# Performance work log

Measured on AMD Instinct MI355X. Metric: run time of the kernel, lower is better.

The kernel has to match this reference:

```python
import jax, jax.numpy as jnp
import numpy as np

T0 = 64    # coarse proposal intervals
TF = 128   # fine samples per ray


def contract(x):
    # mip-NeRF-360 style contraction with per-point max-coordinate scatter.
    ax = jnp.abs(x)
    mag = jnp.max(ax, axis=-1, keepdims=True)             # [..., 1]
    oh = jax.nn.one_hot(jnp.argmax(ax, axis=-1), x.shape[-1], dtype=x.dtype)
    scale = (1.0 - oh) / mag + oh * (2.0 - 1.0 / mag) / mag
    return jnp.where(mag < 1.0, x, x * scale)


def near_far_from_aabb(rays_o, rays_d, aabb, min_near=0.05):
    tmin = (aabb[:3] - rays_o) / (rays_d + 1e-15)
    tmax = (aabb[3:] - rays_o) / (rays_d + 1e-15)
    near = jnp.max(jnp.minimum(tmin, tmax), axis=-1, keepdims=True)
    far = jnp.min(jnp.maximum(tmin, tmax), axis=-1, keepdims=True)
    miss = far < near
    near = jnp.where(miss, 1e9, near)
    far = jnp.where(miss, 1e9, far)
    near = jnp.maximum(near, min_near)
    return near, far


def sample_pdf(bins, weights, T):
    # CDF inverse-transform sampling (no perturb), faithful to the torch helper.
    n_int = weights.shape[-1]
    w = weights + 0.01
    pdf = w / jnp.sum(w, axis=-1, keepdims=True)
    cdf = jnp.minimum(jnp.cumsum(pdf, axis=-1), 1.0)
    cdf = jnp.concatenate([jnp.zeros_like(cdf[..., :1]), cdf], axis=-1)  # [N, n_int+1]
    u = jnp.linspace(0.5 / T, 1.0 - 0.5 / T, T, dtype=bins.dtype)
    u = jnp.broadcast_to(u, (bins.shape[0], T))
    inds = jax.vmap(lambda c, uu: jnp.searchsorted(c, uu, side='right'))(cdf, u)
    below = jnp.clip(inds - 1, 0, n_int)
    above = jnp.clip(inds, 0, n_int)
    cdf0 = jnp.take_along_axis(cdf, below, axis=-1)
    cdf1 = jnp.take_along_axis(cdf, above, axis=-1)
    b0 = jnp.take_along_axis(bins, below, axis=-1)
    b1 = jnp.take_along_axis(bins, above, axis=-1)
    denom = cdf1 - cdf0
    t = jnp.clip(jnp.where(denom > 0, (u - cdf0) / jnp.maximum(denom, 1e-12), 0.0), 0.0, 1.0)
    return b0 + t * (b1 - b0)


def setup_inputs() -> dict:
    key = jax.random.key(0)
    k1, k2, k3, k4, k5 = jax.random.split(key, 5)
    N = 65536
    rays_o = (jax.random.uniform(k1, (N, 3), jnp.float32) - 0.5) * 1.0   # origins inside box
    d = jax.random.normal(k2, (N, 3), jnp.float32)
    rays_d = d / jnp.linalg.norm(d, axis=-1, keepdims=True)
    aabb = jnp.array([-2.0, -2.0, -2.0, 2.0, 2.0, 2.0], jnp.float32)
    weights_coarse = jax.random.uniform(k3, (N, T0), jnp.float32)
    sigmas = jax.random.uniform(k4, (N, TF), jnp.float32) * 20.0
    rgbs = jax.random.uniform(k5, (N, TF, 3), jnp.float32)
    return {"rays_o": rays_o, "rays_d": rays_d, "aabb": aabb,
            "weights_coarse": weights_coarse, "sigmas": sigmas, "rgbs": rgbs}


def reference(rays_o, rays_d, aabb, weights_coarse, sigmas, rgbs):
    N = rays_o.shape[0]
    # 1) ray-AABB intersection
    near, far = near_far_from_aabb(rays_o, rays_d, aabb)
    # 2) uniform coarse bins in [near, far]
    s = jnp.linspace(0.0, 1.0, T0 + 1, dtype=rays_o.dtype)
    bins = near + (far - near) * s                              # [N, T0+1]
    # 3) CDF inverse-sample TF+1 fine bin edges from proposal weights
    z_edges = sample_pdf(bins, weights_coarse, TF + 1)          # [N, TF+1]
    deltas = z_edges[..., 1:] - z_edges[..., :-1]               # [N, TF]
    z = 0.5 * (z_edges[..., 1:] + z_edges[..., :-1])            # [N, TF]
    # 4) sample positions + contraction warp
    xyzs = rays_o[:, None, :] + rays_d[:, None, :] * z[..., None]  # [N, TF, 3]
    xyzs_c = contract(xyzs)
    # 5) alpha compositing
    alphas = 1.0 - jnp.exp(-sigmas * deltas)                    # [N, TF]
    trans = jnp.cumprod(
        jnp.concatenate([jnp.ones_like(alphas[..., :1]), 1.0 - alphas + 1e-10], axis=-1),
        axis=-1)[..., :-1]
    w = alphas * trans                                          # [N, TF]
    image = jnp.sum(w[..., None] * rgbs, axis=1)                # [N, 3]
    depth = jnp.sum(w * z, axis=-1, keepdims=True)              # [N, 1]
    return jnp.concatenate([image, depth, xyzs_c.reshape(N, -1)], axis=-1)  # [N, 4+3*TF]
```

## Files before the change

### kernel.cpp

```cpp
#include <hip/hip_runtime.h>


constexpr int kT0 = 64;
constexpr int kTF = 128;
constexpr int kRaysPerBlock = 4;

template <int Ctrl, int RowMask>
__device__ __forceinline__ float dpp_mov(float x, float oldv) {
    return __int_as_float(__builtin_amdgcn_update_dpp(
        __float_as_int(oldv), __float_as_int(x), Ctrl, RowMask, 0xf, false));
}

__device__ __forceinline__ float wave_iscan_add(float x) {
    x += dpp_mov<0x111, 0xf>(x, 0.0f);
    x += dpp_mov<0x112, 0xf>(x, 0.0f);
    x += dpp_mov<0x114, 0xf>(x, 0.0f);
    x += dpp_mov<0x118, 0xf>(x, 0.0f);
    x += dpp_mov<0x142, 0xa>(x, 0.0f);
    x += dpp_mov<0x143, 0xc>(x, 0.0f);
    return x;
}

__device__ __forceinline__ float wave_iscan_mul(float x) {
    x *= dpp_mov<0x111, 0xf>(x, 1.0f);
    x *= dpp_mov<0x112, 0xf>(x, 1.0f);
    x *= dpp_mov<0x114, 0xf>(x, 1.0f);
    x *= dpp_mov<0x118, 0xf>(x, 1.0f);
    x *= dpp_mov<0x142, 0xa>(x, 1.0f);
    x *= dpp_mov<0x143, 0xc>(x, 1.0f);
    return x;
}

template <int Dummy = 0>
__device__ __forceinline__ float wave_shr1(float x, float oldv) {
    return dpp_mov<0x138, 0xf>(x, oldv);
}

__global__ __launch_bounds__(256)
void nerf_render_kernel(const float* __restrict__ rays_o,
                        const float* __restrict__ rays_d,
                        const float* __restrict__ aabb,
                        const float* __restrict__ weights,
                        const float* __restrict__ sigmas,
                        const float* __restrict__ rgbs,
                        float* __restrict__ out)
{
    const int lane = threadIdx.x & 63;
    const int wid  = threadIdx.x >> 6;
    const int ray  = blockIdx.x * kRaysPerBlock + wid;

    __shared__ float s_zedge[kRaysPerBlock][kTF + 2];

    const float wraw = weights[(size_t)ray * kT0 + lane];
    const float2 sg  = *(const float2*)(sigmas + (size_t)ray * kTF + 2 * lane);
    const float* rgb_row = rgbs + (size_t)ray * (kTF * 3) + 6 * lane;
    const float2 rgA = *(const float2*)(rgb_row + 0);
    const float2 rgB = *(const float2*)(rgb_row + 2);
    const float2 rgC = *(const float2*)(rgb_row + 4);

    const float ox = rays_o[ray * 3 + 0], oy = rays_o[ray * 3 + 1], ozr = rays_o[ray * 3 + 2];
    const float dx = rays_d[ray * 3 + 0], dy = rays_d[ray * 3 + 1], dzr = rays_d[ray * 3 + 2];
    float near, far;
    {
        const float rx = __builtin_amdgcn_rcpf(dx + 1e-15f);
        const float ry = __builtin_amdgcn_rcpf(dy + 1e-15f);
        const float rz = __builtin_amdgcn_rcpf(dzr + 1e-15f);
        const float t0x = (aabb[0] - ox) * rx, t1x = (aabb[3] - ox) * rx;
        const float t0y = (aabb[1] - oy) * ry, t1y = (aabb[4] - oy) * ry;
        const float t0z = (aabb[2] - ozr) * rz, t1z = (aabb[5] - ozr) * rz;
        near = fmaxf(fmaxf(fminf(t0x, t1x), fminf(t0y, t1y)), fminf(t0z, t1z));
        far  = fminf(fminf(fmaxf(t0x, t1x), fmaxf(t0y, t1y)), fmaxf(t0z, t1z));
        if (far < near) { near = 1e9f; far = 1e9f; }
        near = fmaxf(near, 0.05f);
    }
    const float range = far - near;

    const float scan  = wave_iscan_add(wraw + 0.01f);
    const float total = __int_as_float(__builtin_amdgcn_readlane(__float_as_int(scan), 63));
    const float c_hi  = fminf(scan * __builtin_amdgcn_rcpf(total), 1.0f);
    const float c_lo  = wave_shr1<>(c_hi, 0.0f);

    {
        const float b_lo = near + range * ((float)lane * (1.0f / kT0));
        const float bw = range * (1.0f / kT0);
        int j_start = (int)ceilf(fmaf(129.0f, c_lo, -0.5f));
        int j_end   = (int)ceilf(fmaf(129.0f, c_hi, -0.5f));
        j_start = j_start < 0 ? 0 : j_start;
        j_end   = j_end > (kTF + 1) ? (kTF + 1) : j_end;
        const float rdenom = __builtin_amdgcn_rcpf(c_hi - c_lo);
        float fj = (float)j_start + 0.5f;
        for (int j = j_start; j < j_end; ++j, fj += 1.0f) {
            const float u = fj * (1.0f / 129.0f);
            float t = (u - c_lo) * rdenom;
            t = fminf(fmaxf(t, 0.0f), 1.0f);
            s_zedge[wid][j] = fmaf(t, bw, b_lo);
        }
    }
    __builtin_amdgcn_wave_barrier();
    __asm__ volatile("s_waitcnt lgkmcnt(0)" ::: "memory");
    __builtin_amdgcn_wave_barrier();

    const float2 ze01 = *(const float2*)&s_zedge[wid][2 * lane];
    const float  ze2  = s_zedge[wid][2 * lane + 2];
    const float d0 = ze01.y - ze01.x, d1 = ze2 - ze01.y;
    const float z0 = 0.5f * (ze01.x + ze01.y), z1 = 0.5f * (ze01.y + ze2);

    const float e0 = __expf(-sg.x * d0);
    const float e1 = __expf(-sg.y * d1);
    const float a0 = 1.0f - e0, a1 = 1.0f - e1;
    const float f0 = e0 + 1e-10f;
    const float f1 = e1 + 1e-10f;

    const float ps   = wave_iscan_mul(f0 * f1);
    const float excl = wave_shr1<>(ps, 1.0f);
    const float w0 = a0 * excl;
    const float w1 = a1 * excl * f0;

    float vr = wave_iscan_add(w0 * rgA.x + w1 * rgB.y);
    float vg = wave_iscan_add(w0 * rgA.y + w1 * rgC.x);
    float vb = wave_iscan_add(w0 * rgB.x + w1 * rgC.y);
    float vd = wave_iscan_add(w0 * z0 + w1 * z1);

    float* orow = out + (size_t)ray * (4 + kTF * 3);
    if (lane == 63) {
        *(float4*)orow = make_float4(vr, vg, vb, vd);
    }

    float oxyz[6];
    #pragma unroll
    for (int s = 0; s < 2; ++s) {
        const float z = s ? z1 : z0;
        float px = ox  + dx  * z;
        float py = oy  + dy  * z;
        float pz = ozr + dzr * z;
        const float ax = fabsf(px), ay = fabsf(py), az = fabsf(pz);
        float mag; int idx;
        if (ax >= ay && ax >= az) { mag = ax; idx = 0; }
        else if (ay >= az)        { mag = ay; idx = 1; }
        else                      { mag = az; idx = 2; }
        const float inv    = __builtin_amdgcn_rcpf(mag);
        const bool  inside = mag < 1.0f;
        const float s_oth  = inside ? 1.0f : inv;
        const float s_max  = inside ? 1.0f : (2.0f - inv) * inv;
        oxyz[3 * s + 0] = px * ((idx == 0) ? s_max : s_oth);
        oxyz[3 * s + 1] = py * ((idx == 1) ? s_max : s_oth);
        oxyz[3 * s + 2] = pz * ((idx == 2) ? s_max : s_oth);
    }
    float* o = orow + 4 + 6 * lane;
    *(float2*)(o + 0) = make_float2(oxyz[0], oxyz[1]);
    *(float2*)(o + 2) = make_float2(oxyz[2], oxyz[3]);
    *(float2*)(o + 4) = make_float2(oxyz[4], oxyz[5]);
}

extern "C" void kernel_launch(void* const* d_in, const int* in_sizes, int n_in,
                              void* d_out, int out_size, void* d_ws, size_t ws_size,
                              hipStream_t stream) {
    const float* rays_o  = (const float*)d_in[0];
    const float* rays_d  = (const float*)d_in[1];
    const float* aabb    = (const float*)d_in[2];
    const float* weights = (const float*)d_in[3];
    const float* sigmas  = (const float*)d_in[4];
    const float* rgbs    = (const float*)d_in[5];
    float* out           = (float*)d_out;

    const int N = in_sizes[0] / 3;
    const int blocks = N / kRaysPerBlock;
    nerf_render_kernel<<<blocks, 256, 0, stream>>>(rays_o, rays_d, aabb, weights, sigmas, rgbs, out);
}
```

Measured before the change: 221.1 us.

## Process multiple rays per wave with software-prefetched next-ray loads

Each wavefront now handles eight consecutive rays in an unrolled loop, loading the next ray's inputs before processing the current one, with double-buffered LDS z-edge rows. The aim is to hide global memory latency inside each wave and to amortize per-block setup such as the aabb loads. The trade-off is fewer blocks and more registers per thread, with a launch-bounds occupancy hint to keep register use in check. Less parallelism may hurt if occupancy was what hid latency before.

```diff
diff --git a/kernel.cpp b/kernel.cpp
--- a/kernel.cpp
+++ b/kernel.cpp
@@ -3,7 +3,8 @@
 
 constexpr int kT0 = 64;
 constexpr int kTF = 128;
-constexpr int kRaysPerBlock = 4;
+constexpr int kWavesPerBlock = 4;
+constexpr int kRaysPerWave = 8;
 
 template <int Ctrl, int RowMask>
 __device__ __forceinline__ float dpp_mov(float x, float oldv) {
@@ -31,43 +32,48 @@
     return x;
 }
 
-template <int Dummy = 0>
 __device__ __forceinline__ float wave_shr1(float x, float oldv) {
     return dpp_mov<0x138, 0xf>(x, oldv);
 }
 
-__global__ __launch_bounds__(256)
-void nerf_render_kernel(const float* __restrict__ rays_o,
-                        const float* __restrict__ rays_d,
-                        const float* __restrict__ aabb,
-                        const float* __restrict__ weights,
-                        const float* __restrict__ sigmas,
-                        const float* __restrict__ rgbs,
-                        float* __restrict__ out)
-{
-    const int lane = threadIdx.x & 63;
-    const int wid  = threadIdx.x >> 6;
-    const int ray  = blockIdx.x * kRaysPerBlock + wid;
-
-    __shared__ float s_zedge[kRaysPerBlock][kTF + 2];
-
-    const float wraw = weights[(size_t)ray * kT0 + lane];
-    const float2 sg  = *(const float2*)(sigmas + (size_t)ray * kTF + 2 * lane);
+struct RayIn {
+    float ox, oy, oz, dx, dy, dz;
+    float wraw;
+    float2 sg;
+    float2 rgA, rgB, rgC;
+};
+
+__device__ __forceinline__ RayIn load_ray(const float* __restrict__ rays_o,
+                                          const float* __restrict__ rays_d,
+                                          const float* __restrict__ weights,
+                                          const float* __restrict__ sigmas,
+                                          const float* __restrict__ rgbs,
+                                          int ray, int lane) {
+    RayIn r;
+    r.ox = rays_o[ray * 3 + 0]; r.oy = rays_o[ray * 3 + 1]; r.oz = rays_o[ray * 3 + 2];
+    r.dx = rays_d[ray * 3 + 0]; r.dy = rays_d[ray * 3 + 1]; r.dz = rays_d[ray * 3 + 2];
+    r.wraw = weights[(size_t)ray * kT0 + lane];
+    r.sg = *(const float2*)(sigmas + (size_t)ray * kTF + 2 * lane);
     const float* rgb_row = rgbs + (size_t)ray * (kTF * 3) + 6 * lane;
-    const float2 rgA = *(const float2*)(rgb_row + 0);
-    const float2 rgB = *(const float2*)(rgb_row + 2);
-    const float2 rgC = *(const float2*)(rgb_row + 4);
-
-    const float ox = rays_o[ray * 3 + 0], oy = rays_o[ray * 3 + 1], ozr = rays_o[ray * 3 + 2];
-    const float dx = rays_d[ray * 3 + 0], dy = rays_d[ray * 3 + 1], dzr = rays_d[ray * 3 + 2];
+    r.rgA = *(const float2*)(rgb_row + 0);
+    r.rgB = *(const float2*)(rgb_row + 2);
+    r.rgC = *(const float2*)(rgb_row + 4);
+    return r;
+}
+
+__device__ __forceinline__ void process_ray(const RayIn& rin, int ray, int lane,
+                                            float a0, float a1, float a2,
+                                            float a3, float a4, float a5,
+                                            float* __restrict__ zrow,
+                                            float* __restrict__ out) {
     float near, far;
     {
-        const float rx = __builtin_amdgcn_rcpf(dx + 1e-15f);
-        const float ry = __builtin_amdgcn_rcpf(dy + 1e-15f);
-        const float rz = __builtin_amdgcn_rcpf(dzr + 1e-15f);
-        const float t0x = (aabb[0] - ox) * rx, t1x = (aabb[3] - ox) * rx;
-        const float t0y = (aabb[1] - oy) * ry, t1y = (aabb[4] - oy) * ry;
-        const float t0z = (aabb[2] - ozr) * rz, t1z = (aabb[5] - ozr) * rz;
+        const float rx = __builtin_amdgcn_rcpf(rin.dx + 1e-15f);
+        const float ry = __builtin_amdgcn_rcpf(rin.dy + 1e-15f);
+        const float rz = __builtin_amdgcn_rcpf(rin.dz + 1e-15f);
+        const float t0x = (a0 - rin.ox) * rx, t1x = (a3 - rin.ox) * rx;
+        const float t0y = (a1 - rin.oy) * ry, t1y = (a4 - rin.oy) * ry;
+        const float t0z = (a2 - rin.oz) * rz, t1z = (a5 - rin.oz) * rz;
         near = fmaxf(fmaxf(fminf(t0x, t1x), fminf(t0y, t1y)), fminf(t0z, t1z));
         far  = fminf(fminf(fmaxf(t0x, t1x), fmaxf(t0y, t1y)), fmaxf(t0z, t1z));
         if (far < near) { near = 1e9f; far = 1e9f; }
@@ -75,10 +81,10 @@
     }
     const float range = far - near;
 
-    const float scan  = wave_iscan_add(wraw + 0.01f);
+    const float scan  = wave_iscan_add(rin.wraw + 0.01f);
     const float total = __int_as_float(__builtin_amdgcn_readlane(__float_as_int(scan), 63));
     const float c_hi  = fminf(scan * __builtin_amdgcn_rcpf(total), 1.0f);
-    const float c_lo  = wave_shr1<>(c_hi, 0.0f);
+    const float c_lo  = wave_shr1(c_hi, 0.0f);
 
     {
         const float b_lo = near + range * ((float)lane * (1.0f / kT0));
@@ -93,32 +99,32 @@
             const float u = fj * (1.0f / 129.0f);
             float t = (u - c_lo) * rdenom;
             t = fminf(fmaxf(t, 0.0f), 1.0f);
-            s_zedge[wid][j] = fmaf(t, bw, b_lo);
+            zrow[j] = fmaf(t, bw, b_lo);
         }
     }
     __builtin_amdgcn_wave_barrier();
     __asm__ volatile("s_waitcnt lgkmcnt(0)" ::: "memory");
     __builtin_amdgcn_wave_barrier();
 
-    const float2 ze01 = *(const float2*)&s_zedge[wid][2 * lane];
-    const float  ze2  = s_zedge[wid][2 * lane + 2];
+    const float2 ze01 = *(const float2*)&zrow[2 * lane];
+    const float  ze2  = zrow[2 * lane + 2];
     const float d0 = ze01.y - ze01.x, d1 = ze2 - ze01.y;
     const float z0 = 0.5f * (ze01.x + ze01.y), z1 = 0.5f * (ze01.y + ze2);
 
-    const float e0 = __expf(-sg.x * d0);
-    const float e1 = __expf(-sg.y * d1);
-    const float a0 = 1.0f - e0, a1 = 1.0f - e1;
+    const float e0 = __expf(-rin.sg.x * d0);
+    const float e1 = __expf(-rin.sg.y * d1);
+    const float alpha0 = 1.0f - e0, alpha1 = 1.0f - e1;
     const float f0 = e0 + 1e-10f;
     const float f1 = e1 + 1e-10f;
 
     const float ps   = wave_iscan_mul(f0 * f1);
-    const float excl = wave_shr1<>(ps, 1.0f);
-    const float w0 = a0 * excl;
-    const float w1 = a1 * excl * f0;
-
-    float vr = wave_iscan_add(w0 * rgA.x + w1 * rgB.y);
-    float vg = wave_iscan_add(w0 * rgA.y + w1 * rgC.x);
-    float vb = wave_iscan_add(w0 * rgB.x + w1 * rgC.y);
+    const float excl = wave_shr1(ps, 1.0f);
+    const float w0 = alpha0 * excl;
+    const float w1 = alpha1 * excl * f0;
+
+    float vr = wave_iscan_add(w0 * rin.rgA.x + w1 * rin.rgB.y);
+    float vg = wave_iscan_add(w0 * rin.rgA.y + w1 * rin.rgC.x);
+    float vb = wave_iscan_add(w0 * rin.rgB.x + w1 * rin.rgC.y);
     float vd = wave_iscan_add(w0 * z0 + w1 * z1);
 
     float* orow = out + (size_t)ray * (4 + kTF * 3);
@@ -130,9 +136,9 @@
     #pragma unroll
     for (int s = 0; s < 2; ++s) {
         const float z = s ? z1 : z0;
-        float px = ox  + dx  * z;
-        float py = oy  + dy  * z;
-        float pz = ozr + dzr * z;
+        float px = rin.ox + rin.dx * z;
+        float py = rin.oy + rin.dy * z;
+        float pz = rin.oz + rin.dz * z;
         const float ax = fabsf(px), ay = fabsf(py), az = fabsf(pz);
         float mag; int idx;
         if (ax >= ay && ax >= az) { mag = ax; idx = 0; }
@@ -152,6 +158,39 @@
     *(float2*)(o + 4) = make_float2(oxyz[4], oxyz[5]);
 }
 
+__global__ __launch_bounds__(256, 8)
+void nerf_render_kernel(const float* __restrict__ rays_o,
+                        const float* __restrict__ rays_d,
+                        const float* __restrict__ aabb,
+                        const float* __restrict__ weights,
+                        const float* __restrict__ sigmas,
+                        const float* __restrict__ rgbs,
+                        float* __restrict__ out)
+{
+    const int lane = threadIdx.x & 63;
+    const int wid  = threadIdx.x >> 6;
+    const int gw   = blockIdx.x * kWavesPerBlock + wid;
+    const int ray0 = gw * kRaysPerWave;
+
+    __shared__ float s_zedge[2][kWavesPerBlock][kTF + 2];
+
+    const float a0 = aabb[0], a1 = aabb[1], a2 = aabb[2];
+    const float a3 = aabb[3], a4 = aabb[4], a5 = aabb[5];
+
+    RayIn cur = load_ray(rays_o, rays_d, weights, sigmas, rgbs, ray0, lane);
+
+    #pragma unroll
+    for (int t = 0; t < kRaysPerWave; ++t) {
+        RayIn nxt;
+        if (t + 1 < kRaysPerWave) {
+            nxt = load_ray(rays_o, rays_d, weights, sigmas, rgbs, ray0 + t + 1, lane);
+        }
+        process_ray(cur, ray0 + t, lane, a0, a1, a2, a3, a4, a5,
+                    &s_zedge[t & 1][wid][0], out);
+        cur = nxt;
+    }
+}
+
 extern "C" void kernel_launch(void* const* d_in, const int* in_sizes, int n_in,
                               void* d_out, int out_size, void* d_ws, size_t ws_size,
                               hipStream_t stream) {
@@ -164,6 +203,6 @@
     float* out           = (float*)d_out;
 
     const int N = in_sizes[0] / 3;
-    const int blocks = N / kRaysPerBlock;
+    const int blocks = N / (kWavesPerBlock * kRaysPerWave);
     nerf_render_kernel<<<blocks, 256, 0, stream>>>(rays_o, rays_d, aabb, weights, sigmas, rgbs, out);
 }
```

After: 241.1 us. +9.1%, slower.

## Process two rays per wave with interleaved DPP scans for ILP

Applied to the files above, without the earlier changes.

Each wave now handles two rays, one from each half of the batch, and interleaves their loads, CDF scans, transmittance scans and reductions so independent DPP chains can overlap. It also adds a min-blocks hint to launch bounds and halves the grid. The aim is to hide DPP and memory latency through instruction-level parallelism and to issue more loads per wave. The cost is higher register pressure and half as many waves in flight.

```diff
diff --git a/kernel.cpp b/kernel.cpp
--- a/kernel.cpp
+++ b/kernel.cpp
@@ -3,12 +3,30 @@
 
 constexpr int kT0 = 64;
 constexpr int kTF = 128;
-constexpr int kRaysPerBlock = 4;
+constexpr int kWavesPerBlock = 4;
 
 template <int Ctrl, int RowMask>
 __device__ __forceinline__ float dpp_mov(float x, float oldv) {
     return __int_as_float(__builtin_amdgcn_update_dpp(
         __float_as_int(oldv), __float_as_int(x), Ctrl, RowMask, 0xf, false));
+}
+
+__device__ __forceinline__ void wave_iscan_add2(float& a, float& b) {
+    a += dpp_mov<0x111, 0xf>(a, 0.0f);  b += dpp_mov<0x111, 0xf>(b, 0.0f);
+    a += dpp_mov<0x112, 0xf>(a, 0.0f);  b += dpp_mov<0x112, 0xf>(b, 0.0f);
+    a += dpp_mov<0x114, 0xf>(a, 0.0f);  b += dpp_mov<0x114, 0xf>(b, 0.0f);
+    a += dpp_mov<0x118, 0xf>(a, 0.0f);  b += dpp_mov<0x118, 0xf>(b, 0.0f);
+    a += dpp_mov<0x142, 0xa>(a, 0.0f);  b += dpp_mov<0x142, 0xa>(b, 0.0f);
+    a += dpp_mov<0x143, 0xc>(a, 0.0f);  b += dpp_mov<0x143, 0xc>(b, 0.0f);
+}
+
+__device__ __forceinline__ void wave_iscan_mul2(float& a, float& b) {
+    a *= dpp_mov<0x111, 0xf>(a, 1.0f);  b *= dpp_mov<0x111, 0xf>(b, 1.0f);
+    a *= dpp_mov<0x112, 0xf>(a, 1.0f);  b *= dpp_mov<0x112, 0xf>(b, 1.0f);
+    a *= dpp_mov<0x114, 0xf>(a, 1.0f);  b *= dpp_mov<0x114, 0xf>(b, 1.0f);
+    a *= dpp_mov<0x118, 0xf>(a, 1.0f);  b *= dpp_mov<0x118, 0xf>(b, 1.0f);
+    a *= dpp_mov<0x142, 0xa>(a, 1.0f);  b *= dpp_mov<0x142, 0xa>(b, 1.0f);
+    a *= dpp_mov<0x143, 0xc>(a, 1.0f);  b *= dpp_mov<0x143, 0xc>(b, 1.0f);
 }
 
 __device__ __forceinline__ float wave_iscan_add(float x) {
@@ -21,135 +39,192 @@
     return x;
 }
 
-__device__ __forceinline__ float wave_iscan_mul(float x) {
-    x *= dpp_mov<0x111, 0xf>(x, 1.0f);
-    x *= dpp_mov<0x112, 0xf>(x, 1.0f);
-    x *= dpp_mov<0x114, 0xf>(x, 1.0f);
-    x *= dpp_mov<0x118, 0xf>(x, 1.0f);
-    x *= dpp_mov<0x142, 0xa>(x, 1.0f);
-    x *= dpp_mov<0x143, 0xc>(x, 1.0f);
-    return x;
-}
-
-template <int Dummy = 0>
 __device__ __forceinline__ float wave_shr1(float x, float oldv) {
     return dpp_mov<0x138, 0xf>(x, oldv);
 }
 
-__global__ __launch_bounds__(256)
+__global__ __launch_bounds__(256, 8)
 void nerf_render_kernel(const float* __restrict__ rays_o,
                         const float* __restrict__ rays_d,
                         const float* __restrict__ aabb,
                         const float* __restrict__ weights,
                         const float* __restrict__ sigmas,
                         const float* __restrict__ rgbs,
-                        float* __restrict__ out)
+                        float* __restrict__ out,
+                        int Nh)
 {
     const int lane = threadIdx.x & 63;
     const int wid  = threadIdx.x >> 6;
-    const int ray  = blockIdx.x * kRaysPerBlock + wid;
-
-    __shared__ float s_zedge[kRaysPerBlock][kTF + 2];
-
-    const float wraw = weights[(size_t)ray * kT0 + lane];
-    const float2 sg  = *(const float2*)(sigmas + (size_t)ray * kTF + 2 * lane);
-    const float* rgb_row = rgbs + (size_t)ray * (kTF * 3) + 6 * lane;
-    const float2 rgA = *(const float2*)(rgb_row + 0);
-    const float2 rgB = *(const float2*)(rgb_row + 2);
-    const float2 rgC = *(const float2*)(rgb_row + 4);
-
-    const float ox = rays_o[ray * 3 + 0], oy = rays_o[ray * 3 + 1], ozr = rays_o[ray * 3 + 2];
-    const float dx = rays_d[ray * 3 + 0], dy = rays_d[ray * 3 + 1], dzr = rays_d[ray * 3 + 2];
-    float near, far;
-    {
-        const float rx = __builtin_amdgcn_rcpf(dx + 1e-15f);
-        const float ry = __builtin_amdgcn_rcpf(dy + 1e-15f);
-        const float rz = __builtin_amdgcn_rcpf(dzr + 1e-15f);
-        const float t0x = (aabb[0] - ox) * rx, t1x = (aabb[3] - ox) * rx;
-        const float t0y = (aabb[1] - oy) * ry, t1y = (aabb[4] - oy) * ry;
-        const float t0z = (aabb[2] - ozr) * rz, t1z = (aabb[5] - ozr) * rz;
-        near = fmaxf(fmaxf(fminf(t0x, t1x), fminf(t0y, t1y)), fminf(t0z, t1z));
-        far  = fminf(fminf(fmaxf(t0x, t1x), fmaxf(t0y, t1y)), fmaxf(t0z, t1z));
-        if (far < near) { near = 1e9f; far = 1e9f; }
-        near = fmaxf(near, 0.05f);
-    }
-    const float range = far - near;
-
-    const float scan  = wave_iscan_add(wraw + 0.01f);
-    const float total = __int_as_float(__builtin_amdgcn_readlane(__float_as_int(scan), 63));
-    const float c_hi  = fminf(scan * __builtin_amdgcn_rcpf(total), 1.0f);
-    const float c_lo  = wave_shr1<>(c_hi, 0.0f);
-
-    {
-        const float b_lo = near + range * ((float)lane * (1.0f / kT0));
-        const float bw = range * (1.0f / kT0);
-        int j_start = (int)ceilf(fmaf(129.0f, c_lo, -0.5f));
-        int j_end   = (int)ceilf(fmaf(129.0f, c_hi, -0.5f));
+    const int gw   = blockIdx.x * kWavesPerBlock + wid;
+    const int rayA = gw;
+    const int rayB = gw + Nh;
+
+    __shared__ float s_zedge[kWavesPerBlock][2][kTF + 2];
+
+    const float oxA = rays_o[rayA * 3 + 0], oyA = rays_o[rayA * 3 + 1], ozA = rays_o[rayA * 3 + 2];
+    const float dxA = rays_d[rayA * 3 + 0], dyA = rays_d[rayA * 3 + 1], dzA = rays_d[rayA * 3 + 2];
+    const float oxB = rays_o[rayB * 3 + 0], oyB = rays_o[rayB * 3 + 1], ozB = rays_o[rayB * 3 + 2];
+    const float dxB = rays_d[rayB * 3 + 0], dyB = rays_d[rayB * 3 + 1], dzB = rays_d[rayB * 3 + 2];
+    const float wrawA = weights[(size_t)rayA * kT0 + lane];
+    const float wrawB = weights[(size_t)rayB * kT0 + lane];
+    const float2 sgA = *(const float2*)(sigmas + (size_t)rayA * kTF + 2 * lane);
+    const float2 sgB = *(const float2*)(sigmas + (size_t)rayB * kTF + 2 * lane);
+    const float* rgbA = rgbs + (size_t)rayA * (kTF * 3) + 6 * lane;
+    const float* rgbB = rgbs + (size_t)rayB * (kTF * 3) + 6 * lane;
+    const float2 rgA0 = *(const float2*)(rgbA + 0);
+    const float2 rgA1 = *(const float2*)(rgbA + 2);
+    const float2 rgA2 = *(const float2*)(rgbA + 4);
+    const float2 rgB0 = *(const float2*)(rgbB + 0);
+    const float2 rgB1 = *(const float2*)(rgbB + 2);
+    const float2 rgB2 = *(const float2*)(rgbB + 4);
+
+    const float a0 = aabb[0], a1 = aabb[1], a2 = aabb[2];
+    const float a3 = aabb[3], a4 = aabb[4], a5 = aabb[5];
+
+    float nearA, farA, nearB, farB;
+    {
+        const float rx = __builtin_amdgcn_rcpf(dxA + 1e-15f);
+        const float ry = __builtin_amdgcn_rcpf(dyA + 1e-15f);
+        const float rz = __builtin_amdgcn_rcpf(dzA + 1e-15f);
+        const float t0x = (a0 - oxA) * rx, t1x = (a3 - oxA) * rx;
+        const float t0y = (a1 - oyA) * ry, t1y = (a4 - oyA) * ry;
+        const float t0z = (a2 - ozA) * rz, t1z = (a5 - ozA) * rz;
+        nearA = fmaxf(fmaxf(fminf(t0x, t1x), fminf(t0y, t1y)), fminf(t0z, t1z));
+        farA  = fminf(fminf(fmaxf(t0x, t1x), fmaxf(t0y, t1y)), fmaxf(t0z, t1z));
+        if (farA < nearA) { nearA = 1e9f; farA = 1e9f; }
+        nearA = fmaxf(nearA, 0.05f);
+    }
+    {
+        const float rx = __builtin_amdgcn_rcpf(dxB + 1e-15f);
+        const float ry = __builtin_amdgcn_rcpf(dyB + 1e-15f);
+        const float rz = __builtin_amdgcn_rcpf(dzB + 1e-15f);
+        const float t0x = (a0 - oxB) * rx, t1x = (a3 - oxB) * rx;
+        const float t0y = (a1 - oyB) * ry, t1y = (a4 - oyB) * ry;
+        const float t0z = (a2 - ozB) * rz, t1z = (a5 - ozB) * rz;
+        nearB = fmaxf(fmaxf(fminf(t0x, t1x), fminf(t0y, t1y)), fminf(t0z, t1z));
+        farB  = fminf(fminf(fmaxf(t0x, t1x), fmaxf(t0y, t1y)), fmaxf(t0z, t1z));
+        if (farB < nearB) { nearB = 1e9f; farB = 1e9f; }
+        nearB = fmaxf(nearB, 0.05f);
+    }
+    const float rangeA = farA - nearA;
+    const float rangeB = farB - nearB;
+
+    float scanA = wrawA + 0.01f, scanB = wrawB + 0.01f;
+    wave_iscan_add2(scanA, scanB);
+    const float totA = __int_as_float(__builtin_amdgcn_readlane(__float_as_int(scanA), 63));
+    const float totB = __int_as_float(__builtin_amdgcn_readlane(__float_as_int(scanB), 63));
+    const float c_hiA = fminf(scanA * __builtin_amdgcn_rcpf(totA), 1.0f);
+    const float c_hiB = fminf(scanB * __builtin_amdgcn_rcpf(totB), 1.0f);
+    const float c_loA = wave_shr1(c_hiA, 0.0f);
+    const float c_loB = wave_shr1(c_hiB, 0.0f);
+
+    {
+        const float b_lo = nearA + rangeA * ((float)lane * (1.0f / kT0));
+        const float bw = rangeA * (1.0f / kT0);
+        int j_start = (int)ceilf(fmaf(129.0f, c_loA, -0.5f));
+        int j_end   = (int)ceilf(fmaf(129.0f, c_hiA, -0.5f));
         j_start = j_start < 0 ? 0 : j_start;
         j_end   = j_end > (kTF + 1) ? (kTF + 1) : j_end;
-        const float rdenom = __builtin_amdgcn_rcpf(c_hi - c_lo);
+        const float rdenom = __builtin_amdgcn_rcpf(c_hiA - c_loA);
         float fj = (float)j_start + 0.5f;
         for (int j = j_start; j < j_end; ++j, fj += 1.0f) {
-            const float u = fj * (1.0f / 129.0f);
-            float t = (u - c_lo) * rdenom;
+            float t = (fj * (1.0f / 129.0f) - c_loA) * rdenom;
             t = fminf(fmaxf(t, 0.0f), 1.0f);
-            s_zedge[wid][j] = fmaf(t, bw, b_lo);
+            s_zedge[wid][0][j] = fmaf(t, bw, b_lo);
+        }
+    }
+    {
+        const float b_lo = nearB + rangeB * ((float)lane * (1.0f / kT0));
+        const float bw = rangeB * (1.0f / kT0);
+        int j_start = (int)ceilf(fmaf(129.0f, c_loB, -0.5f));
+        int j_end   = (int)ceilf(fmaf(129.0f, c_hiB, -0.5f));
+        j_start = j_start < 0 ? 0 : j_start;
+        j_end   = j_end > (kTF + 1) ? (kTF + 1) : j_end;
+        const float rdenom = __builtin_amdgcn_rcpf(c_hiB - c_loB);
+        float fj = (float)j_start + 0.5f;
+        for (int j = j_start; j < j_end; ++j, fj += 1.0f) {
+            float t = (fj * (1.0f / 129.0f) - c_loB) * rdenom;
+            t = fminf(fmaxf(t, 0.0f), 1.0f);
+            s_zedge[wid][1][j] = fmaf(t, bw, b_lo);
         }
     }
     __builtin_amdgcn_wave_barrier();
     __asm__ volatile("s_waitcnt lgkmcnt(0)" ::: "memory");
     __builtin_amdgcn_wave_barrier();
 
-    const float2 ze01 = *(const float2*)&s_zedge[wid][2 * lane];
-    const float  ze2  = s_zedge[wid][2 * lane + 2];
-    const float d0 = ze01.y - ze01.x, d1 = ze2 - ze01.y;
-    const float z0 = 0.5f * (ze01.x + ze01.y), z1 = 0.5f * (ze01.y + ze2);
-
-    const float e0 = __expf(-sg.x * d0);
-    const float e1 = __expf(-sg.y * d1);
-    const float a0 = 1.0f - e0, a1 = 1.0f - e1;
-    const float f0 = e0 + 1e-10f;
-    const float f1 = e1 + 1e-10f;
-
-    const float ps   = wave_iscan_mul(f0 * f1);
-    const float excl = wave_shr1<>(ps, 1.0f);
-    const float w0 = a0 * excl;
-    const float w1 = a1 * excl * f0;
-
-    float vr = wave_iscan_add(w0 * rgA.x + w1 * rgB.y);
-    float vg = wave_iscan_add(w0 * rgA.y + w1 * rgC.x);
-    float vb = wave_iscan_add(w0 * rgB.x + w1 * rgC.y);
-    float vd = wave_iscan_add(w0 * z0 + w1 * z1);
-
-    float* orow = out + (size_t)ray * (4 + kTF * 3);
+    const float2 zeA01 = *(const float2*)&s_zedge[wid][0][2 * lane];
+    const float  zeA2  = s_zedge[wid][0][2 * lane + 2];
+    const float2 zeB01 = *(const float2*)&s_zedge[wid][1][2 * lane];
+    const float  zeB2  = s_zedge[wid][1][2 * lane + 2];
+    const float d0A = zeA01.y - zeA01.x, d1A = zeA2 - zeA01.y;
+    const float z0A = 0.5f * (zeA01.x + zeA01.y), z1A = 0.5f * (zeA01.y + zeA2);
+    const float d0B = zeB01.y - zeB01.x, d1B = zeB2 - zeB01.y;
+    const float z0B = 0.5f * (zeB01.x + zeB01.y), z1B = 0.5f * (zeB01.y + zeB2);
+
+    const float e0A = __expf(-sgA.x * d0A), e1A = __expf(-sgA.y * d1A);
+    const float e0B = __expf(-sgB.x * d0B), e1B = __expf(-sgB.y * d1B);
+    const float al0A = 1.0f - e0A, al1A = 1.0f - e1A;
+    const float al0B = 1.0f - e0B, al1B = 1.0f - e1B;
+    const float f0A = e0A + 1e-10f, f1A = e1A + 1e-10f;
+    const float f0B = e0B + 1e-10f, f1B = e1B + 1e-10f;
+
+    float psA = f0A * f1A, psB = f0B * f1B;
+    wave_iscan_mul2(psA, psB);
+    const float exclA = wave_shr1(psA, 1.0f);
+    const float exclB = wave_shr1(psB, 1.0f);
+    const float w0A = al0A * exclA, w1A = al1A * exclA * f0A;
+    const float w0B = al0B * exclB, w1B = al1B * exclB * f0B;
+
+    float vrA = w0A * rgA0.x + w1A * rgA1.y;
+    float vgA = w0A * rgA0.y + w1A * rgA2.x;
+    float vbA = w0A * rgA1.x + w1A * rgA2.y;
+    float vdA = w0A * z0A + w1A * z1A;
+    float vrB = w0B * rgB0.x + w1B * rgB1.y;
+    float vgB = w0B * rgB0.y + w1B * rgB2.x;
+    float vbB = w0B * rgB1.x + w1B * rgB2.y;
+    float vdB = w0B * z0B + w1B * z1B;
+    wave_iscan_add2(vrA, vrB);
+    wave_iscan_add2(vgA, vgB);
+    wave_iscan_add2(vbA, vbB);
+    wave_iscan_add2(vdA, vdB);
+
+    float* orowA = out + (size_t)rayA * (4 + kTF * 3);
+    float* orowB = out + (size_t)rayB * (4 + kTF * 3);
     if (lane == 63) {
-        *(float4*)orow = make_float4(vr, vg, vb, vd);
-    }
-
-    float oxyz[6];
+        *(float4*)orowA = make_float4(vrA, vgA, vbA, vdA);
+        *(float4*)orowB = make_float4(vrB, vgB, vbB, vdB);
+    }
+
     #pragma unroll
-    for (int s = 0; s < 2; ++s) {
-        const float z = s ? z1 : z0;
-        float px = ox  + dx  * z;
-        float py = oy  + dy  * z;
-        float pz = ozr + dzr * z;
-        const float ax = fabsf(px), ay = fabsf(py), az = fabsf(pz);
-        float mag; int idx;
-        if (ax >= ay && ax >= az) { mag = ax; idx = 0; }
-        else if (ay >= az)        { mag = ay; idx = 1; }
-        else                      { mag = az; idx = 2; }
-        const float inv    = __builtin_amdgcn_rcpf(mag);
-        const bool  inside = mag < 1.0f;
-        const float s_oth  = inside ? 1.0f : inv;
-        const float s_max  = inside ? 1.0f : (2.0f - inv) * inv;
-        oxyz[3 * s + 0] = px * ((idx == 0) ? s_max : s_oth);
-        oxyz[3 * s + 1] = py * ((idx == 1) ? s_max : s_oth);
-        oxyz[3 * s + 2] = pz * ((idx == 2) ? s_max : s_oth);
-    }
-    float* o = orow + 4 + 6 * lane;
-    *(float2*)(o + 0) = make_float2(oxyz[0], oxyz[1]);
-    *(float2*)(o + 2) = make_float2(oxyz[2], oxyz[3]);
-    *(float2*)(o + 4) = make_float2(oxyz[4], oxyz[5]);
+    for (int r = 0; r < 2; ++r) {
+        const float ox = r ? oxB : oxA, oy = r ? oyB : oyA, oz = r ? ozB : ozA;
+        const float dx = r ? dxB : dxA, dy = r ? dyB : dyA, dz = r ? dzB : dzA;
+        const float z0 = r ? z0B : z0A, z1 = r ? z1B : z1A;
+        float oxyz[6];
+        #pragma unroll
+        for (int s = 0; s < 2; ++s) {
+            const float z = s ? z1 : z0;
+            float px = ox + dx * z;
+            float py = oy + dy * z;
+            float pz = oz + dz * z;
+            const float ax = fabsf(px), ay = fabsf(py), az = fabsf(pz);
+            float mag; int idx;
+            if (ax >= ay && ax >= az) { mag = ax; idx = 0; }
+            else if (ay >= az)        { mag = ay; idx = 1; }
+            else                      { mag = az; idx = 2; }
+            const float inv    = __builtin_amdgcn_rcpf(mag);
+            const bool  inside = mag < 1.0f;
+            const float s_oth  = inside ? 1.0f : inv;
+            const float s_max  = inside ? 1.0f : (2.0f - inv) * inv;
+            oxyz[3 * s + 0] = px * ((idx == 0) ? s_max : s_oth);
+            oxyz[3 * s + 1] = py * ((idx == 1) ? s_max : s_oth);
+            oxyz[3 * s + 2] = pz * ((idx == 2) ? s_max : s_oth);
+        }
+        float* o = (r ? orowB : orowA) + 4 + 6 * lane;
+        *(float2*)(o + 0) = make_float2(oxyz[0], oxyz[1]);
+        *(float2*)(o + 2) = make_float2(oxyz[2], oxyz[3]);
+        *(float2*)(o + 4) = make_float2(oxyz[4], oxyz[5]);
+    }
 }
 
 extern "C" void kernel_launch(void* const* d_in, const int* in_sizes, int n_in,
@@ -164,6 +239,7 @@
     float* out           = (float*)d_out;
 
     const int N = in_sizes[0] / 3;
-    const int blocks = N / kRaysPerBlock;
-    nerf_render_kernel<<<blocks, 256, 0, stream>>>(rays_o, rays_d, aabb, weights, sigmas, rgbs, out);
-}
+    const int Nh = N / 2;
+    const int blocks = Nh / kWavesPerBlock;
+    nerf_render_kernel<<<blocks, 256, 0, stream>>>(rays_o, rays_d, aabb, weights, sigmas, rgbs, out, Nh);
+}
```

Result: no change. 222.9 us (+0.8%).
